# Kernel tuning notes

Hardware: AMD Instinct MI355X
Metric: run time of the kernel (lower is better)

## Reference

```python
import jax, jax.numpy as jnp
import numpy as np

N, IN_C, HID, OUT_C, DEPTH = 4096, 128, 256, 128, 3
KS = [2048, 1024, 512]  # ceil(0.5 * N_level)
E = 131072


def glorot(key, fan_in, fan_out):
    lim = np.sqrt(6.0 / (fan_in + fan_out))
    return jax.random.uniform(key, (fan_in, fan_out), jnp.float32, -lim, lim)


def build_adj(edge_index, n):
    # symmetric, self-loop-free adjacency with unit edge weights
    A = jnp.zeros((n, n), jnp.float32)
    A = A.at[edge_index[0], edge_index[1]].set(1.0)
    A = jnp.maximum(A, A.T)
    return A * (1.0 - jnp.eye(n, dtype=jnp.float32))


def gcn(x, A, W, b):
    # GCNConv(improved=True): A_hat = A + 2I, symmetric normalization
    n = A.shape[0]
    Ah = A + 2.0 * jnp.eye(n, dtype=A.dtype)
    deg = Ah.sum(axis=1)
    dinv = jnp.where(deg > 0, deg ** -0.5, 0.0)
    An = dinv[:, None] * Ah * dinv[None, :]
    return An @ (x @ W) + b


def augment(A):
    # remove self loops, add self loops (w=1), square (spspmm), remove self loops
    n = A.shape[0]
    I = jnp.eye(n, dtype=A.dtype)
    Al = A * (1.0 - I) + I
    A2 = Al @ Al
    return A2 * (1.0 - I)


def topk_pool(x, A, p, k):
    score = jnp.tanh((x @ p) / jnp.linalg.norm(p))
    vals, perm = jax.lax.top_k(score, k)
    return x[perm] * vals[:, None], A[perm][:, perm], perm


def setup_inputs() -> dict:
    key = jax.random.key(0)
    ks = jax.random.split(key, 16)
    x = jax.random.normal(ks[0], (N, IN_C), jnp.float32)
    edge_index = jax.random.randint(ks[1], (2, E), 0, N, jnp.int32)
    d = {"x": x, "edge_index": edge_index}
    d["Wd0"], d["bd0"] = glorot(ks[2], IN_C, HID), jnp.zeros((HID,), jnp.float32)
    d["Wd1"], d["bd1"] = glorot(ks[3], HID, HID), jnp.zeros((HID,), jnp.float32)
    d["Wd2"], d["bd2"] = glorot(ks[4], HID, HID), jnp.zeros((HID,), jnp.float32)
    d["Wd3"], d["bd3"] = glorot(ks[5], HID, HID), jnp.zeros((HID,), jnp.float32)
    d["p1"] = jax.random.normal(ks[6], (HID,), jnp.float32)
    d["p2"] = jax.random.normal(ks[7], (HID,), jnp.float32)
    d["p3"] = jax.random.normal(ks[8], (HID,), jnp.float32)
    d["Wu0"], d["bu0"] = glorot(ks[9], HID, HID), jnp.zeros((HID,), jnp.float32)
    d["Wu1"], d["bu1"] = glorot(ks[10], HID, HID), jnp.zeros((HID,), jnp.float32)
    d["Wu2"], d["bu2"] = glorot(ks[11], HID, OUT_C), jnp.zeros((OUT_C,), jnp.float32)
    return d


def reference(x, edge_index, Wd0, bd0, Wd1, bd1, Wd2, bd2, Wd3, bd3,
              p1, p2, p3, Wu0, bu0, Wu1, bu1, Wu2, bu2):
    n = x.shape[0]
    A = build_adj(edge_index, n)
    x = jax.nn.relu(gcn(x, A, Wd0, bd0))
    xs, As, perms = [x], [A], []
    down = [(Wd1, bd1), (Wd2, bd2), (Wd3, bd3)]
    pools = [p1, p2, p3]
    for i in range(DEPTH):
        A = augment(A)
        x, A, perm = topk_pool(x, A, pools[i], KS[i])
        x = jax.nn.relu(gcn(x, A, *down[i]))
        if i < DEPTH - 1:
            xs.append(x)
            As.append(A)
        perms.append(perm)
    up = [(Wu0, bu0), (Wu1, bu1), (Wu2, bu2)]
    for i in range(DEPTH):
        j = DEPTH - 1 - i
        res, perm = xs[j], perms[j]
        u = jnp.zeros_like(res).at[perm].set(x)
        x = res + u  # sum_res=True
        x = gcn(x, As[j], *up[i])
        if i < DEPTH - 1:
            x = jax.nn.relu(x)
    return x
```

## Files before the change

### kernel.cpp

```cpp
#include <hip/hip_runtime.h>


typedef __attribute__((ext_vector_type(8))) short bf16x8;
typedef __attribute__((ext_vector_type(4))) short s16x4;
typedef __attribute__((ext_vector_type(4))) float f32x4;

__device__ __forceinline__ short f2bf(float f) {
    unsigned u = __builtin_bit_cast(unsigned, f);
    u += 0x7FFFu + ((u >> 16) & 1u);
    return (short)(u >> 16);
}
__device__ __forceinline__ float bf2f(short s) {
    unsigned u = ((unsigned)(unsigned short)s) << 16;
    return __builtin_bit_cast(float, u);
}

#define GLL16(gsrc, ldst)                                                        \
    __builtin_amdgcn_global_load_lds(                                            \
        (__attribute__((address_space(1))) void*)(gsrc),                         \
        (__attribute__((address_space(3))) void*)(ldst), 16, 0, 0)

template<int MODE, int EPI>
__global__ __launch_bounds__(256, 2)
void gemm_bt(const short* __restrict__ Ah, const short* __restrict__ Al,
             const short* __restrict__ Bh, const short* __restrict__ Bl,
             float* __restrict__ Cf, int M, int N, int K, int kChunk)
{
    if (EPI == 1 && (int)blockIdx.y > (int)blockIdx.x) return;

    __shared__ short sAh[128 * 32];
    __shared__ short sBh[128 * 32];
    __shared__ short sAl[(MODE == 2) ? 128 * 32 : 8];
    __shared__ short sBl[(MODE >= 1) ? 128 * 32 : 8];

    const int t    = threadIdx.x;
    const int lane = t & 63;
    const int wave = t >> 6;
    const int tM   = blockIdx.y * 128;
    const int tN   = blockIdx.x * 128;
    const int k0   = blockIdx.z * kChunk;

    const int wm  = (wave >> 1) * 64;
    const int wn  = (wave & 1) * 64;
    const int l15 = lane & 15;
    const int g8  = (lane >> 4) * 8;

    f32x4 acc[4][4];
    const f32x4 zero = {0.f, 0.f, 0.f, 0.f};
#pragma unroll
    for (int i = 0; i < 4; i++)
#pragma unroll
        for (int j = 0; j < 4; j++) acc[i][j] = zero;

    const int i0 = t, i1 = t + 256;
    const short* a0 = Ah + (size_t)(tM + (i0 >> 2)) * K + (i0 & 3) * 8;
    const short* a1 = Ah + (size_t)(tM + (i1 >> 2)) * K + (i1 & 3) * 8;
    const short* b0 = Bh + (size_t)(tN + (i0 >> 2)) * K + (i0 & 3) * 8;
    const short* b1 = Bh + (size_t)(tN + (i1 >> 2)) * K + (i1 & 3) * 8;
    const short *bl0 = nullptr, *bl1 = nullptr, *al0 = nullptr, *al1 = nullptr;
    if (MODE >= 1) {
        bl0 = Bl + (size_t)(tN + (i0 >> 2)) * K + (i0 & 3) * 8;
        bl1 = Bl + (size_t)(tN + (i1 >> 2)) * K + (i1 & 3) * 8;
    }
    if (MODE == 2) {
        al0 = Al + (size_t)(tM + (i0 >> 2)) * K + (i0 & 3) * 8;
        al1 = Al + (size_t)(tM + (i1 >> 2)) * K + (i1 & 3) * 8;
    }

    for (int kb = k0; kb < k0 + kChunk; kb += 32) {
        GLL16(a0 + kb, &sAh[i0 * 8]);
        GLL16(a1 + kb, &sAh[i1 * 8]);
        GLL16(b0 + kb, &sBh[i0 * 8]);
        GLL16(b1 + kb, &sBh[i1 * 8]);
        if (MODE >= 1) { GLL16(bl0 + kb, &sBl[i0 * 8]); GLL16(bl1 + kb, &sBl[i1 * 8]); }
        if (MODE == 2) { GLL16(al0 + kb, &sAl[i0 * 8]); GLL16(al1 + kb, &sAl[i1 * 8]); }
        __syncthreads();

        bf16x8 aF[4], bF[4], aL[4], bL[4];
#pragma unroll
        for (int i = 0; i < 4; i++)
            aF[i] = *(const bf16x8*)&sAh[(wm + i * 16 + l15) * 32 + g8];
#pragma unroll
        for (int j = 0; j < 4; j++)
            bF[j] = *(const bf16x8*)&sBh[(wn + j * 16 + l15) * 32 + g8];
        if (MODE >= 1)
#pragma unroll
            for (int j = 0; j < 4; j++)
                bL[j] = *(const bf16x8*)&sBl[(wn + j * 16 + l15) * 32 + g8];
        if (MODE == 2)
#pragma unroll
            for (int i = 0; i < 4; i++)
                aL[i] = *(const bf16x8*)&sAl[(wm + i * 16 + l15) * 32 + g8];

#pragma unroll
        for (int i = 0; i < 4; i++)
#pragma unroll
            for (int j = 0; j < 4; j++) {
                acc[i][j] = __builtin_amdgcn_mfma_f32_16x16x32_bf16(aF[i], bF[j], acc[i][j], 0, 0, 0);
                if (MODE >= 1)
                    acc[i][j] = __builtin_amdgcn_mfma_f32_16x16x32_bf16(aF[i], bL[j], acc[i][j], 0, 0, 0);
                if (MODE == 2)
                    acc[i][j] = __builtin_amdgcn_mfma_f32_16x16x32_bf16(aL[i], bF[j], acc[i][j], 0, 0, 0);
            }
        __syncthreads();
    }

    const int r4 = (lane >> 4) * 4;
    if (EPI == 3) {
        float* CT = Cf + (size_t)blockIdx.z * M * N;
#pragma unroll
        for (int i = 0; i < 4; i++)
#pragma unroll
            for (int j = 0; j < 4; j++) {
                const int col   = tN + wn + j * 16 + l15;
                const int rbase = tM + wm + i * 16 + r4;
                *(f32x4*)&CT[(size_t)col * M + rbase] = acc[i][j];
            }
    } else {
        float* Cg = Cf + (size_t)blockIdx.z * M * N;
#pragma unroll
        for (int i = 0; i < 4; i++)
#pragma unroll
            for (int j = 0; j < 4; j++) {
                const int col = tN + wn + j * 16 + l15;
                float* cp = Cg + (size_t)(tM + wm + i * 16 + r4) * N + col;
#pragma unroll
                for (int r = 0; r < 4; r++) cp[(size_t)r * N] = acc[i][j][r];
            }
        if (EPI == 1 && tM != tN) {
#pragma unroll
            for (int i = 0; i < 4; i++)
#pragma unroll
                for (int j = 0; j < 4; j++) {
                    const int col   = tN + wn + j * 16 + l15;
                    const int rbase = tM + wm + i * 16 + r4;
                    *(f32x4*)&Cg[(size_t)col * N + rbase] = acc[i][j];
                }
        }
    }
}


__global__ void prep(const float* __restrict__ Wd0, const float* __restrict__ Wd1,
                     const float* __restrict__ Wd2, const float* __restrict__ Wd3,
                     const float* __restrict__ Wu0, const float* __restrict__ Wu1,
                     const float* __restrict__ Wu2, const float* __restrict__ x0,
                     short* __restrict__ Wth, short* __restrict__ Wtl,
                     short* __restrict__ Xh, short* __restrict__ Xl,
                     unsigned long long* __restrict__ M0)
{
    int t = blockIdx.x * 256 + threadIdx.x;
    float v; int dst;
    if (t < 32768)       { int e = t;          v = Wd0[e]; dst = 0      + (e & 255) * 128 + (e >> 8); }
    else if (t < 98304)  { int e = t - 32768;  v = Wd1[e]; dst = 32768  + (e & 255) * 256 + (e >> 8); }
    else if (t < 163840) { int e = t - 98304;  v = Wd2[e]; dst = 98304  + (e & 255) * 256 + (e >> 8); }
    else if (t < 229376) { int e = t - 163840; v = Wd3[e]; dst = 163840 + (e & 255) * 256 + (e >> 8); }
    else if (t < 294912) { int e = t - 229376; v = Wu0[e]; dst = 229376 + (e & 255) * 256 + (e >> 8); }
    else if (t < 360448) { int e = t - 294912; v = Wu1[e]; dst = 294912 + (e & 255) * 256 + (e >> 8); }
    else if (t < 393216) { int e = t - 360448; v = Wu2[e]; dst = 360448 + (e & 127) * 256 + (e >> 7); }
    else if (t < 917504) {
        int e = t - 393216;
        v = x0[e];
        short h = f2bf(v);
        Xh[e] = h; Xl[e] = f2bf(v - bf2f(h));
        return;
    } else {
        M0[t - 917504] = 0ull;
        return;
    }
    short h = f2bf(v);
    Wth[dst] = h; Wtl[dst] = f2bf(v - bf2f(h));
}

__global__ void build_bits(const int* __restrict__ ei, int E,
                           unsigned long long* __restrict__ M0)
{
    int e = blockIdx.x * 256 + threadIdx.x;
    if (e >= E) return;
    int i = ei[e], j = ei[E + e];
    if (i != j) {
        atomicOr(&M0[(size_t)i * 64 + (j >> 6)], 1ull << (j & 63));
        atomicOr(&M0[(size_t)j * 64 + (i >> 6)], 1ull << (i & 63));
    }
}

__global__ void row_compact_bits(const unsigned long long* __restrict__ M0,
                                 int* __restrict__ csr, float* __restrict__ rs)
{
    int row = blockIdx.x * 4 + (threadIdx.x >> 6);
    int lane = threadIdx.x & 63;
    unsigned long long w = M0[(size_t)row * 64 + lane];
    int c = __popcll(w);
    int incl = c;
    for (int off = 1; off < 64; off <<= 1) {
        int v = __shfl_up(incl, off);
        if (lane >= off) incl += v;
    }
    int base = incl - c;
    int* out = csr + (size_t)row * 128;
    while (w) {
        int b = __ffsll((unsigned long long)w) - 1;
        if (base < 128) out[base] = lane * 64 + b;
        base++;
        w &= w - 1;
    }
    if (lane == 63) rs[row] = (float)incl;
}

__global__ void mask_gather(const unsigned long long* __restrict__ M0,
                            const int* __restrict__ perm,
                            unsigned long long* __restrict__ mask,
                            float* __restrict__ rs, int kk)
{
    int t = blockIdx.x * 256 + threadIdx.x;
    if (t < kk) rs[t] = 0.f;
    int r = t >> 6, l = t & 63;
    int u = perm[r];
    unsigned long long w = M0[(size_t)u * 64 + l];
    if ((u >> 6) == l) w |= 1ull << (u & 63);
    mask[t] = w;
}

#define PSTR2 18
__global__ __launch_bounds__(256, 8)
void popc_aug_p(const unsigned long long* __restrict__ mask,
                short* __restrict__ Cp)
{
    const int bx = blockIdx.x, by = blockIdx.y, z = blockIdx.z;
    if (by > bx) return;
    __shared__ unsigned long long a[64 * PSTR2];
    __shared__ unsigned long long b[64 * PSTR2];
    const int t = threadIdx.x;
#pragma unroll
    for (int p = 0; p < 4; p++) {
        int idx = p * 256 + t;
        int rr = idx >> 4, w = idx & 15;
        a[rr * PSTR2 + w] = mask[((size_t)(by * 64 + rr)) * 64 + z * 16 + w];
        b[rr * PSTR2 + w] = mask[((size_t)(bx * 64 + rr)) * 64 + z * 16 + w];
    }
    __syncthreads();
    const int i0 = (t >> 4) * 4;
    const int j0 = t & 15;
    int acc[4][4];
#pragma unroll
    for (int qi = 0; qi < 4; qi++)
#pragma unroll
        for (int qj = 0; qj < 4; qj++) acc[qi][qj] = 0;
#pragma unroll
    for (int w = 0; w < 16; w += 2) {
        ulong2 av[4], bv[4];
#pragma unroll
        for (int q = 0; q < 4; q++) av[q] = *(const ulong2*)&a[(i0 + q) * PSTR2 + w];
#pragma unroll
        for (int q = 0; q < 4; q++) bv[q] = *(const ulong2*)&b[(j0 + 16 * q) * PSTR2 + w];
#pragma unroll
        for (int qi = 0; qi < 4; qi++)
#pragma unroll
            for (int qj = 0; qj < 4; qj++) {
                acc[qi][qj] += __builtin_popcountll(av[qi].x & bv[qj].x);
                acc[qi][qj] += __builtin_popcountll(av[qi].y & bv[qj].y);
            }
    }
    short* out = Cp + ((size_t)z * 1024 + (size_t)(by * 32 + bx)) * 4096;
#pragma unroll
    for (int qi = 0; qi < 4; qi++)
#pragma unroll
        for (int qj = 0; qj < 4; qj++)
            out[(i0 + qi) * 64 + j0 + 16 * qj] = (short)acc[qi][qj];
}

__global__ __launch_bounds__(256)
void aug_merge(const short* __restrict__ Cp, int kk,
               short* __restrict__ Ahs, float* __restrict__ rs)
{
    const int bx = blockIdx.x, by = blockIdx.y;
    if (by > bx) return;
    __shared__ float tile[64][65];
    __shared__ float rsum[64], csum[64];
    const int t = threadIdx.x;
    const int i  = t >> 2;
    const int c0 = (t & 3) * 16;
    const size_t tb = (size_t)(by * 32 + bx) * 4096;
    const size_t ss = (size_t)1024 * 4096;
    if (t < 64) { rsum[t] = 0.f; csum[t] = 0.f; }

    int v[16];
#pragma unroll
    for (int q = 0; q < 16; q++) v[q] = 0;
    for (int s = 0; s < 4; s++) {
        bf16x8 p0 = *(const bf16x8*)&Cp[tb + s * ss + i * 64 + c0];
        bf16x8 p1 = *(const bf16x8*)&Cp[tb + s * ss + i * 64 + c0 + 8];
#pragma unroll
        for (int q = 0; q < 8; q++) { v[q] += (int)p0[q]; v[8 + q] += (int)p1[q]; }
    }
    const int gi = by * 64 + i;
    float rp = 0.f;
    s16x4 pk[4];
#pragma unroll
    for (int q = 0; q < 16; q++) {
        const int gj = bx * 64 + c0 + q;
        float val = (gi == gj) ? 0.f : (float)v[q];
        tile[i][c0 + q] = val;
        rp += val;
        pk[q >> 2][q & 3] = f2bf(val);
    }
#pragma unroll
    for (int q = 0; q < 4; q++)
        *(s16x4*)&Ahs[(size_t)gi * kk + bx * 64 + c0 + q * 4] = pk[q];
    __syncthreads();
    atomicAdd(&rsum[i], rp);
    if (bx != by) {
        float cpv = 0.f;
#pragma unroll
        for (int q = 0; q < 16; q++) {
            float val = tile[c0 + q][i];
            cpv += val;
            pk[q >> 2][q & 3] = f2bf(val);
        }
#pragma unroll
        for (int q = 0; q < 4; q++)
            *(s16x4*)&Ahs[(size_t)(bx * 64 + i) * kk + by * 64 + c0 + q * 4] = pk[q];
        atomicAdd(&csum[i], cpv);
    }
    __syncthreads();
    if (t < 64) {
        atomicAdd(&rs[by * 64 + t], rsum[t]);
        if (bx != by) atomicAdd(&rs[bx * 64 + t], csum[t]);
    }
}

__global__ void z_reduce(const float* __restrict__ Cp, int S,
                         const float* __restrict__ rs,
                         short* __restrict__ Zh, short* __restrict__ Zl,
                         int n, int C)
{
    int t4 = (blockIdx.x * 256 + threadIdx.x) * 4;
    int r = t4 % n;
    size_t stride = (size_t)n * C;
    f32x4 v = {0.f, 0.f, 0.f, 0.f};
    for (int s = 0; s < S; s++) v += *(const f32x4*)&Cp[t4 + s * stride];
    f32x4 rsv = *(const f32x4*)&rs[r];
    s16x4 zh, zl;
#pragma unroll
    for (int q = 0; q < 4; q++) {
        float z = v[q] / sqrtf(rsv[q] + 2.f);
        short h = f2bf(z);
        zh[q] = h; zl[q] = f2bf(z - bf2f(h));
    }
    *(s16x4*)&Zh[t4] = zh;
    *(s16x4*)&Zl[t4] = zl;
}

__global__ void zf_reduce(const float* __restrict__ Cp, int S,
                          const float* __restrict__ rs,
                          float* __restrict__ Zf, int n, int C)
{
    int t4 = (blockIdx.x * 256 + threadIdx.x) * 4;
    int r = t4 / C;
    size_t stride = (size_t)n * C;
    f32x4 v = {0.f, 0.f, 0.f, 0.f};
    for (int s = 0; s < S; s++) v += *(const f32x4*)&Cp[t4 + s * stride];
    float d = 1.f / sqrtf(rs[r] + 2.f);
    v *= d;
    *(f32x4*)&Zf[t4] = v;
}

template<int CN, int RELU>
__global__ __launch_bounds__(256)
void spmm_gcn(const int* __restrict__ csr, const float* __restrict__ rs,
              const float* __restrict__ Zf, const float* __restrict__ b,
              float* __restrict__ out)
{
    const int lane = threadIdx.x & 63;
    const int row  = blockIdx.x * 4 + (threadIdx.x >> 6);
    const int dg   = (int)rs[row];
    const int* nb  = csr + (size_t)row * 128;
    if (CN == 256) {
        const int c = lane * 4;
        float4 acc = {0.f, 0.f, 0.f, 0.f};
        int q = 0;
        for (; q + 4 <= dg; q += 4) {
            int j0 = nb[q], j1 = nb[q+1], j2 = nb[q+2], j3 = nb[q+3];
            float4 z0 = *(const float4*)&Zf[(size_t)j0 * CN + c];
            float4 z1 = *(const float4*)&Zf[(size_t)j1 * CN + c];
            float4 z2 = *(const float4*)&Zf[(size_t)j2 * CN + c];
            float4 z3 = *(const float4*)&Zf[(size_t)j3 * CN + c];
            acc.x += z0.x; acc.y += z0.y; acc.z += z0.z; acc.w += z0.w;
            acc.x += z1.x; acc.y += z1.y; acc.z += z1.z; acc.w += z1.w;
            acc.x += z2.x; acc.y += z2.y; acc.z += z2.z; acc.w += z2.w;
            acc.x += z3.x; acc.y += z3.y; acc.z += z3.z; acc.w += z3.w;
        }
        for (; q < dg; q++) {
            float4 z = *(const float4*)&Zf[(size_t)nb[q] * CN + c];
            acc.x += z.x; acc.y += z.y; acc.z += z.z; acc.w += z.w;
        }
        float d = 1.f / sqrtf(rs[row] + 2.f);
        float4 zi = *(const float4*)&Zf[(size_t)row * CN + c];
        float4 bb = *(const float4*)&b[c];
        float4 g;
        g.x = d * acc.x + 2.f * d * zi.x + bb.x;
        g.y = d * acc.y + 2.f * d * zi.y + bb.y;
        g.z = d * acc.z + 2.f * d * zi.z + bb.z;
        g.w = d * acc.w + 2.f * d * zi.w + bb.w;
        if (RELU) {
            g.x = fmaxf(g.x, 0.f); g.y = fmaxf(g.y, 0.f);
            g.z = fmaxf(g.z, 0.f); g.w = fmaxf(g.w, 0.f);
        }
        *(float4*)&out[(size_t)row * CN + c] = g;
    } else {
        const int c = lane * 2;
        float2 acc = {0.f, 0.f};
        int q = 0;
        for (; q + 4 <= dg; q += 4) {
            int j0 = nb[q], j1 = nb[q+1], j2 = nb[q+2], j3 = nb[q+3];
            float2 z0 = *(const float2*)&Zf[(size_t)j0 * CN + c];
            float2 z1 = *(const float2*)&Zf[(size_t)j1 * CN + c];
            float2 z2 = *(const float2*)&Zf[(size_t)j2 * CN + c];
            float2 z3 = *(const float2*)&Zf[(size_t)j3 * CN + c];
            acc.x += z0.x; acc.y += z0.y;
            acc.x += z1.x; acc.y += z1.y;
            acc.x += z2.x; acc.y += z2.y;
            acc.x += z3.x; acc.y += z3.y;
        }
        for (; q < dg; q++) {
            float2 z = *(const float2*)&Zf[(size_t)nb[q] * CN + c];
            acc.x += z.x; acc.y += z.y;
        }
        float d = 1.f / sqrtf(rs[row] + 2.f);
        float2 zi = *(const float2*)&Zf[(size_t)row * CN + c];
        float2 g;
        g.x = d * acc.x + 2.f * d * zi.x + b[c];
        g.y = d * acc.y + 2.f * d * zi.y + b[c + 1];
        if (RELU) { g.x = fmaxf(g.x, 0.f); g.y = fmaxf(g.y, 0.f); }
        *(float2*)&out[(size_t)row * CN + c] = g;
    }
}

__global__ void gcn_final(const float* __restrict__ Cp, int S,
                          const short* __restrict__ Zh, const short* __restrict__ Zl,
                          const float* __restrict__ rs, const float* __restrict__ b,
                          float* __restrict__ out, short* __restrict__ oh,
                          short* __restrict__ ol, int k, int C, int relu,
                          const int* __restrict__ inv, const float* __restrict__ res)
{
    int t4 = (blockIdx.x * 256 + threadIdx.x) * 4;
    int j = t4 / C, c = t4 - j * C;
    int r = inv ? inv[j] : j;
    f32x4 v = res ? *(const f32x4*)&res[t4] : (f32x4){0.f, 0.f, 0.f, 0.f};
    if (r >= 0) {
        size_t base = (size_t)r * C + c;
        size_t stride = (size_t)k * C;
        f32x4 az = {0.f, 0.f, 0.f, 0.f};
        for (int s = 0; s < S; s++) az += *(const f32x4*)&Cp[base + s * stride];
        float d = 1.f / sqrtf(rs[r] + 2.f);
        f32x4 bb = *(const f32x4*)&b[c];
#pragma unroll
        for (int q = 0; q < 4; q++) {
            size_t zi = (size_t)(c + q) * k + r;
            float zz = bf2f(Zh[zi]) + bf2f(Zl[zi]);
            float g = d * az[q] + 2.f * d * zz + bb[q];
            if (relu && g < 0.f) g = 0.f;
            v[q] += g;
        }
    }
    *(f32x4*)&out[t4] = v;
    if (oh) {
        s16x4 hh, ll;
#pragma unroll
        for (int q = 0; q < 4; q++) {
            short h = f2bf(v[q]);
            hh[q] = h; ll[q] = f2bf(v[q] - bf2f(h));
        }
        *(s16x4*)&oh[t4] = hh;
        *(s16x4*)&ol[t4] = ll;
    }
}

__global__ void score_kernel(const float* __restrict__ x,
                             const float* __restrict__ p,
                             float* __restrict__ score, int n,
                             int* __restrict__ rankb)
{
    int row = blockIdx.x * 4 + (threadIdx.x >> 6);
    int lane = threadIdx.x & 63;
    float4 pv = ((const float4*)p)[lane];
    float4 xv = ((const float4*)(x + (size_t)row * 256))[lane];
    double nn  = (double)pv.x * pv.x + (double)pv.y * pv.y +
                 (double)pv.z * pv.z + (double)pv.w * pv.w;
    double acc = (double)xv.x * pv.x + (double)xv.y * pv.y +
                 (double)xv.z * pv.z + (double)xv.w * pv.w;
    for (int off = 32; off; off >>= 1) {
        acc += __shfl_down(acc, off);
        nn  += __shfl_down(nn, off);
    }
    if (lane == 0) {
        score[row] = tanhf((float)(acc / sqrt(nn)));
        rankb[row] = 0;
    }
}

__device__ __forceinline__ unsigned long long packkey(float s, int i) {
    unsigned u = __builtin_bit_cast(unsigned, s);
    u = (u & 0x80000000u) ? ~u : (u | 0x80000000u);
    return ((unsigned long long)u << 32) | (unsigned)(0xFFFFFFFFu - (unsigned)i);
}

__global__ __launch_bounds__(256)
void rank_count(const float* __restrict__ score,
                int* __restrict__ rankb)
{
    __shared__ unsigned long long sk[256];
    int i = blockIdx.x * 256 + threadIdx.x;
    int j = blockIdx.y * 256 + threadIdx.x;
    sk[threadIdx.x] = packkey(score[j], j);
    unsigned long long mykey = packkey(score[i], i);
    __syncthreads();
    int part = 0;
#pragma unroll 16
    for (int q = 0; q < 256; q++) part += (sk[q] > mykey) ? 1 : 0;
    atomicAdd(&rankb[i], part);
}

__global__ void rank_final(const float* __restrict__ score,
                           const int* __restrict__ rankb, int k,
                           int* __restrict__ perm, float* __restrict__ vals,
                           int* __restrict__ inv)
{
    int i = blockIdx.x * 256 + threadIdx.x;
    int rank = rankb[i];
    if (rank < k) { perm[rank] = i; vals[rank] = score[i]; }
    inv[i] = (rank < k) ? rank : -1;
}

__global__ void gather_x_hl(const float* __restrict__ xold,
                            const int* __restrict__ perm,
                            const float* __restrict__ vals,
                            short* __restrict__ Xh, short* __restrict__ Xl, int C)
{
    int t4 = (blockIdx.x * 256 + threadIdx.x) * 4;
    int r = t4 / C, c = t4 - r * C;
    float vv = vals[r];
    f32x4 x = *(const f32x4*)&xold[(size_t)perm[r] * C + c];
    s16x4 hh, ll;
#pragma unroll
    for (int q = 0; q < 4; q++) {
        float v = x[q] * vv;
        short h = f2bf(v);
        hh[q] = h; ll[q] = f2bf(v - bf2f(h));
    }
    *(s16x4*)&Xh[t4] = hh;
    *(s16x4*)&Xl[t4] = ll;
}

__global__ void gatherG_h(const short* __restrict__ A, int n,
                          const int* __restrict__ perm,
                          short* __restrict__ Gh, int kk,
                          float* __restrict__ rsz)
{
    int idx = blockIdx.x * 256 + threadIdx.x;
    if (idx < kk) rsz[idx] = 0.f;
    int t8 = idx * 8;
    if (t8 >= kk * n) return;
    int r = t8 / n, c0 = t8 - r * n;
    int pr = perm[r];
    bf16x8 a = *(const bf16x8*)&A[(size_t)pr * n + c0];
    if (pr >= c0 && pr < c0 + 8)
        a[pr - c0] = f2bf(bf2f(a[pr - c0]) + 1.f);
    *(bf16x8*)&Gh[t8] = a;
}

__global__ void gatherG_hl(const short* __restrict__ Ahi, const short* __restrict__ Alo,
                           int n, const int* __restrict__ perm,
                           short* __restrict__ Gh, short* __restrict__ Gl, int kk,
                           float* __restrict__ rsz)
{
    int idx = blockIdx.x * 256 + threadIdx.x;
    if (idx < kk) rsz[idx] = 0.f;
    int t8 = idx * 8;
    if (t8 >= kk * n) return;
    int r = t8 / n, c0 = t8 - r * n;
    int pr = perm[r];
    bf16x8 ah = *(const bf16x8*)&Ahi[(size_t)pr * n + c0];
    bf16x8 al = *(const bf16x8*)&Alo[(size_t)pr * n + c0];
    bf16x8 gh, gl;
#pragma unroll
    for (int q = 0; q < 8; q++) {
        float v = bf2f(ah[q]) + bf2f(al[q]) + ((c0 + q == pr) ? 1.f : 0.f);
        short h = f2bf(v);
        gh[q] = h; gl[q] = f2bf(v - bf2f(h));
    }
    *(bf16x8*)&Gh[t8] = gh;
    *(bf16x8*)&Gl[t8] = gl;
}

template<bool LO>
__global__ void aug_finish_f(const float* __restrict__ Cp, int S, int kk,
                             short* __restrict__ Ahs, short* __restrict__ Als,
                             float* __restrict__ rs)
{
    int t4 = (blockIdx.x * 256 + threadIdx.x) * 4;
    int r = t4 / kk, c0 = t4 - r * kk;
    size_t stride = (size_t)kk * kk;
    f32x4 v = {0.f, 0.f, 0.f, 0.f};
    for (int s = 0; s < S; s++) v += *(const f32x4*)&Cp[t4 + s * stride];
    if (r >= c0 && r < c0 + 4) v[r - c0] = 0.f;
    s16x4 hh, ll;
    float ws = 0.f;
#pragma unroll
    for (int q = 0; q < 4; q++) {
        short h = f2bf(v[q]);
        hh[q] = h;
        if (LO) ll[q] = f2bf(v[q] - bf2f(h));
        ws += v[q];
    }
    *(s16x4*)&Ahs[t4] = hh;
    if (LO) *(s16x4*)&Als[t4] = ll;
    for (int off = 32; off; off >>= 1) ws += __shfl_down(ws, off);
    if ((threadIdx.x & 63) == 0) atomicAdd(&rs[r], ws);
}


extern "C" void kernel_launch(void* const* d_in, const int* in_sizes, int n_in,
                              void* d_out, int out_size, void* d_ws, size_t ws_size,
                              hipStream_t stream)
{
    const float* x0  = (const float*)d_in[0];
    const int*   ei  = (const int*)d_in[1];
    const float* Wd0 = (const float*)d_in[2];  const float* bd0 = (const float*)d_in[3];
    const float* Wd1 = (const float*)d_in[4];  const float* bd1 = (const float*)d_in[5];
    const float* Wd2 = (const float*)d_in[6];  const float* bd2 = (const float*)d_in[7];
    const float* Wd3 = (const float*)d_in[8];  const float* bd3 = (const float*)d_in[9];
    const float* p1  = (const float*)d_in[10];
    const float* p2  = (const float*)d_in[11];
    const float* p3  = (const float*)d_in[12];
    const float* Wu0 = (const float*)d_in[13]; const float* bu0 = (const float*)d_in[14];
    const float* Wu1 = (const float*)d_in[15]; const float* bu1 = (const float*)d_in[16];
    const float* Wu2 = (const float*)d_in[17]; const float* bu2 = (const float*)d_in[18];

    const int E = in_sizes[1] / 2;

    char* ws = (char*)d_ws;
    size_t off = 0;
    auto alloc = [&](size_t bytes) -> void* {
        void* p = ws + off;
        off += (bytes + 255) & ~(size_t)255;
        return p;
    };
    unsigned long long* M0 = (unsigned long long*)alloc((size_t)4096 * 64 * 8);
    short* A1h  = (short*)alloc((size_t)2048 * 2048 * 2);
    short* A2h  = (short*)alloc((size_t)1024 * 1024 * 2);
    short* A2l  = (short*)alloc((size_t)1024 * 1024 * 2);
    short* A3h  = (short*)alloc((size_t)512 * 512 * 2);
    short* A3l  = (short*)alloc((size_t)512 * 512 * 2);
    short* Gh   = (short*)alloc((size_t)1024 * 2048 * 2);
    short* Gl   = (short*)alloc((size_t)512 * 1024 * 2);
    int*   csr  = (int*)alloc((size_t)4096 * 128 * 4);
    unsigned long long* maskb = (unsigned long long*)alloc((size_t)2048 * 64 * 8);
    float* Zf   = (float*)alloc((size_t)4096 * 256 * 4);
    float* Cp   = (float*)alloc((size_t)64 * 1024 * 1024);
    float* xs0  = (float*)alloc((size_t)4096 * 256 * 4);
    float* xs1  = (float*)alloc((size_t)2048 * 256 * 4);
    float* xs2  = (float*)alloc((size_t)1024 * 256 * 4);
    float* xu0  = (float*)alloc((size_t)4096 * 256 * 4);
    float* xu1  = (float*)alloc((size_t)2048 * 256 * 4);
    float* xu2  = (float*)alloc((size_t)1024 * 256 * 4);
    short* xu0h = (short*)alloc((size_t)4096 * 256 * 2);
    short* xu0l = (short*)alloc((size_t)4096 * 256 * 2);
    short* xu1h = (short*)alloc((size_t)2048 * 256 * 2);
    short* xu1l = (short*)alloc((size_t)2048 * 256 * 2);
    short* xu2h = (short*)alloc((size_t)1024 * 256 * 2);
    short* xu2l = (short*)alloc((size_t)1024 * 256 * 2);
    short* X0h  = (short*)alloc((size_t)4096 * 128 * 2);
    short* X0l  = (short*)alloc((size_t)4096 * 128 * 2);
    short* xah  = (short*)alloc((size_t)2048 * 256 * 2);
    short* xal  = (short*)alloc((size_t)2048 * 256 * 2);
    short* Wth  = (short*)alloc((size_t)393216 * 2);
    short* Wtl  = (short*)alloc((size_t)393216 * 2);
    short* Zh   = (short*)alloc((size_t)256 * 4096 * 2);
    short* Zl   = (short*)alloc((size_t)256 * 4096 * 2);
    float* rs0  = (float*)alloc(4096 * 4);
    float* rs1  = (float*)alloc(2048 * 4);
    float* rs2  = (float*)alloc(1024 * 4);
    float* rs3  = (float*)alloc(512 * 4);
    float* scoreb = (float*)alloc(4096 * 4);
    float* valsb  = (float*)alloc(2048 * 4);
    int*   rankb  = (int*)alloc(4096 * 4);
    int*   perm1  = (int*)alloc(2048 * 4);
    int*   perm2  = (int*)alloc(1024 * 4);
    int*   perm3  = (int*)alloc(512 * 4);
    int*   inv1   = (int*)alloc(4096 * 4);
    int*   inv2   = (int*)alloc(2048 * 4);
    int*   inv3   = (int*)alloc(1024 * 4);

    auto gcn_dense = [&](const short* Xh, const short* Xl, int n, int Kc, int Cout,
                         const short* pAh, const short* pAl, const float* rsA,
                         int wtoff, const float* b,
                         float* out, short* oh, short* ol, int relu, int modeA,
                         int Saz, const int* inv, const float* res, int nout) {
        int Sxw = 4;
        gemm_bt<2, 3><<<dim3(Cout / 128, n / 128, Sxw), 256, 0, stream>>>(
            Xh, Xl, Wth + wtoff, Wtl + wtoff, Cp, n, Cout, Kc, Kc / Sxw);
        z_reduce<<<(n * Cout) / 1024, 256, 0, stream>>>(Cp, Sxw, rsA, Zh, Zl, n, Cout);
        dim3 g(Cout / 128, n / 128, Saz);
        if (modeA == 1)
            gemm_bt<1, 0><<<g, 256, 0, stream>>>(pAh, nullptr, Zh, Zl, Cp, n, Cout, n, n / Saz);
        else
            gemm_bt<2, 0><<<g, 256, 0, stream>>>(pAh, pAl, Zh, Zl, Cp, n, Cout, n, n / Saz);
        gcn_final<<<(nout * Cout) / 1024, 256, 0, stream>>>(
            Cp, Saz, Zh, Zl, rsA, b, out, oh, ol, n, Cout, relu, inv, res);
    };

    auto pool = [&](const float* xlev, int n, const float* p, int* perm, int* inv) {
        int k = n / 2;
        score_kernel<<<n / 4, 256, 0, stream>>>(xlev, p, scoreb, n, rankb);
        rank_count<<<dim3(n / 256, n / 256), 256, 0, stream>>>(scoreb, rankb);
        rank_final<<<n / 256, 256, 0, stream>>>(scoreb, rankb, k, perm, valsb, inv);
        gather_x_hl<<<k / 4, 256, 0, stream>>>(xlev, perm, valsb, xah, xal, 256);
    };

    prep<<<4608, 256, 0, stream>>>(Wd0, Wd1, Wd2, Wd3, Wu0, Wu1, Wu2, x0,
                                   Wth, Wtl, X0h, X0l, M0);
    build_bits<<<(E + 255) / 256, 256, 0, stream>>>(ei, E, M0);
    row_compact_bits<<<1024, 256, 0, stream>>>(M0, csr, rs0);

    gemm_bt<2, 0><<<dim3(2, 32, 4), 256, 0, stream>>>(
        X0h, X0l, Wth, Wtl, Cp, 4096, 256, 128, 32);
    zf_reduce<<<1024, 256, 0, stream>>>(Cp, 4, rs0, Zf, 4096, 256);
    spmm_gcn<256, 1><<<1024, 256, 0, stream>>>(csr, rs0, Zf, bd0, xs0);

    pool(xs0, 4096, p1, perm1, inv1);
    mask_gather<<<512, 256, 0, stream>>>(M0, perm1, maskb, rs1, 2048);
    popc_aug_p<<<dim3(32, 32, 4), 256, 0, stream>>>(maskb, (short*)Cp);
    aug_merge<<<dim3(32, 32), 256, 0, stream>>>((const short*)Cp, 2048, A1h, rs1);
    gcn_dense(xah, xal, 2048, 256, 256, A1h, nullptr, rs1, 32768, bd1,
              xs1, nullptr, nullptr, 1, 1, 8, nullptr, nullptr, 2048);

    pool(xs1, 2048, p2, perm2, inv2);
    gatherG_h<<<(1024 * 2048 / 8) / 256, 256, 0, stream>>>(A1h, 2048, perm2, Gh, 1024, rs2);
    gemm_bt<0, 1><<<dim3(8, 8, 8), 256, 0, stream>>>(Gh, nullptr, Gh, nullptr, Cp, 1024, 1024, 2048, 256);
    aug_finish_f<true><<<(1024 * 1024 / 4) / 256, 256, 0, stream>>>(Cp, 8, 1024, A2h, A2l, rs2);
    gcn_dense(xah, xal, 1024, 256, 256, A2h, A2l, rs2, 98304, bd2,
              xs2, nullptr, nullptr, 1, 2, 8, nullptr, nullptr, 1024);

    pool(xs2, 1024, p3, perm3, inv3);
    gatherG_hl<<<(512 * 1024 / 8) / 256, 256, 0, stream>>>(A2h, A2l, 1024, perm3, Gh, Gl, 512, rs3);
    gemm_bt<2, 1><<<dim3(4, 4, 8), 256, 0, stream>>>(Gh, Gl, Gh, Gl, Cp, 512, 512, 1024, 128);
    aug_finish_f<true><<<(512 * 512 / 4) / 256, 256, 0, stream>>>(Cp, 8, 512, A3h, A3l, rs3);

    gcn_dense(xah, xal, 512, 256, 256, A3h, A3l, rs3, 163840, bd3,
              xu2, xu2h, xu2l, 1, 2, 8, inv3, xs2, 1024);

    gcn_dense(xu2h, xu2l, 1024, 256, 256, A2h, A2l, rs2, 229376, bu0,
              xu1, xu1h, xu1l, 1, 2, 8, inv2, xs1, 2048);

    gcn_dense(xu1h, xu1l, 2048, 256, 256, A1h, nullptr, rs1, 294912, bu1,
              xu0, xu0h, xu0l, 1, 1, 8, inv1, xs0, 4096);

    gemm_bt<2, 0><<<dim3(1, 32, 8), 256, 0, stream>>>(
        xu0h, xu0l, Wth + 360448, Wtl + 360448, Cp, 4096, 128, 256, 32);
    zf_reduce<<<512, 256, 0, stream>>>(Cp, 8, rs0, Zf, 4096, 128);
    spmm_gcn<128, 0><<<1024, 256, 0, stream>>>(csr, rs0, Zf, bu2, (float*)d_out);
}
```

Measured before the change: 447.6 us.

## Fuse pooling score into GCN epilogues and merge rank/gather into one kernel

The tanh(x·p/|p|) score is now computed in the epilogue of the GCN kernel that produces each level's features (spmm_gcn and gcn_final), which removes the separate score kernel and a re-read of x. The rank-count, rank-final and gather kernels are merged into one rank_pool kernel. Each block ranks 64 nodes by scanning all scores through shared memory, then gathers and splits the selected rows into bf16 hi/lo parts. This cuts three kernel launches per pooling level and drops the rank/vals buffers and global atomics. The cost is that each block redundantly scans all n scores, and there are fewer blocks (n/64).

```diff
diff --git a/kernel.cpp b/kernel.cpp
--- a/kernel.cpp
+++ b/kernel.cpp
@@ -365,11 +365,12 @@
     *(f32x4*)&Zf[t4] = v;
 }
 
-template<int CN, int RELU>
+template<int CN, int RELU, int SC>
 __global__ __launch_bounds__(256)
 void spmm_gcn(const int* __restrict__ csr, const float* __restrict__ rs,
               const float* __restrict__ Zf, const float* __restrict__ b,
-              float* __restrict__ out)
+              float* __restrict__ out,
+              const float* __restrict__ pvec, float* __restrict__ score)
 {
     const int lane = threadIdx.x & 63;
     const int row  = blockIdx.x * 4 + (threadIdx.x >> 6);
@@ -407,6 +408,18 @@
             g.z = fmaxf(g.z, 0.f); g.w = fmaxf(g.w, 0.f);
         }
         *(float4*)&out[(size_t)row * CN + c] = g;
+        if (SC) {
+            float4 pv = ((const float4*)pvec)[lane];
+            double nn  = (double)pv.x * pv.x + (double)pv.y * pv.y +
+                         (double)pv.z * pv.z + (double)pv.w * pv.w;
+            double acd = (double)g.x * pv.x + (double)g.y * pv.y +
+                         (double)g.z * pv.z + (double)g.w * pv.w;
+            for (int off = 32; off; off >>= 1) {
+                acd += __shfl_down(acd, off);
+                nn  += __shfl_down(nn, off);
+            }
+            if (lane == 0) score[row] = tanhf((float)(acd / sqrt(nn)));
+        }
     } else {
         const int c = lane * 2;
         float2 acc = {0.f, 0.f};
@@ -441,7 +454,8 @@
                           const float* __restrict__ rs, const float* __restrict__ b,
                           float* __restrict__ out, short* __restrict__ oh,
                           short* __restrict__ ol, int k, int C, int relu,
-                          const int* __restrict__ inv, const float* __restrict__ res)
+                          const int* __restrict__ inv, const float* __restrict__ res,
+                          const float* __restrict__ pvec, float* __restrict__ score)
 {
     int t4 = (blockIdx.x * 256 + threadIdx.x) * 4;
     int j = t4 / C, c = t4 - j * C;
@@ -474,28 +488,18 @@
         *(s16x4*)&oh[t4] = hh;
         *(s16x4*)&ol[t4] = ll;
     }
-}
-
-__global__ void score_kernel(const float* __restrict__ x,
-                             const float* __restrict__ p,
-                             float* __restrict__ score, int n,
-                             int* __restrict__ rankb)
-{
-    int row = blockIdx.x * 4 + (threadIdx.x >> 6);
-    int lane = threadIdx.x & 63;
-    float4 pv = ((const float4*)p)[lane];
-    float4 xv = ((const float4*)(x + (size_t)row * 256))[lane];
-    double nn  = (double)pv.x * pv.x + (double)pv.y * pv.y +
-                 (double)pv.z * pv.z + (double)pv.w * pv.w;
-    double acc = (double)xv.x * pv.x + (double)xv.y * pv.y +
-                 (double)xv.z * pv.z + (double)xv.w * pv.w;
-    for (int off = 32; off; off >>= 1) {
-        acc += __shfl_down(acc, off);
-        nn  += __shfl_down(nn, off);
-    }
-    if (lane == 0) {
-        score[row] = tanhf((float)(acc / sqrt(nn)));
-        rankb[row] = 0;
+    if (pvec) {
+        const int lane = threadIdx.x & 63;
+        float4 pv = *(const float4*)&pvec[c];
+        double nn  = (double)pv.x * pv.x + (double)pv.y * pv.y +
+                     (double)pv.z * pv.z + (double)pv.w * pv.w;
+        double acd = (double)v[0] * pv.x + (double)v[1] * pv.y +
+                     (double)v[2] * pv.z + (double)v[3] * pv.w;
+        for (int off = 32; off; off >>= 1) {
+            acd += __shfl_down(acd, off);
+            nn  += __shfl_down(nn, off);
+        }
+        if (lane == 0) score[j] = tanhf((float)(acd / sqrt(nn)));
     }
 }
 
@@ -506,50 +510,64 @@
 }
 
 __global__ __launch_bounds__(256)
-void rank_count(const float* __restrict__ score,
-                int* __restrict__ rankb)
+void rank_pool(const float* __restrict__ score, int n, int k,
+               const float* __restrict__ xold,
+               int* __restrict__ perm, int* __restrict__ inv,
+               short* __restrict__ Xh, short* __restrict__ Xl)
 {
     __shared__ unsigned long long sk[256];
-    int i = blockIdx.x * 256 + threadIdx.x;
-    int j = blockIdx.y * 256 + threadIdx.x;
-    sk[threadIdx.x] = packkey(score[j], j);
-    unsigned long long mykey = packkey(score[i], i);
+    __shared__ int rk[64];
+    __shared__ int selrow[64];
+    __shared__ int selrank[64];
+    __shared__ float selval[64];
+    __shared__ int cnt;
+    const int t  = threadIdx.x;
+    const int il = t & 63;
+    const int js = t >> 6;
+    const int i  = blockIdx.x * 64 + il;
+    if (t < 64) rk[t] = 0;
+    if (t == 0) cnt = 0;
+    const unsigned long long mykey = packkey(score[i], i);
+    int r = 0;
+    for (int jb = 0; jb < n; jb += 256) {
+        __syncthreads();
+        sk[t] = packkey(score[jb + t], jb + t);
+        __syncthreads();
+        const unsigned long long* p = &sk[js * 64];
+#pragma unroll 16
+        for (int q = 0; q < 64; q++) r += (p[q] > mykey) ? 1 : 0;
+    }
+    atomicAdd(&rk[il], r);
     __syncthreads();
-    int part = 0;
-#pragma unroll 16
-    for (int q = 0; q < 256; q++) part += (sk[q] > mykey) ? 1 : 0;
-    atomicAdd(&rankb[i], part);
-}
-
-__global__ void rank_final(const float* __restrict__ score,
-                           const int* __restrict__ rankb, int k,
-                           int* __restrict__ perm, float* __restrict__ vals,
-                           int* __restrict__ inv)
-{
-    int i = blockIdx.x * 256 + threadIdx.x;
-    int rank = rankb[i];
-    if (rank < k) { perm[rank] = i; vals[rank] = score[i]; }
-    inv[i] = (rank < k) ? rank : -1;
-}
-
-__global__ void gather_x_hl(const float* __restrict__ xold,
-                            const int* __restrict__ perm,
-                            const float* __restrict__ vals,
-                            short* __restrict__ Xh, short* __restrict__ Xl, int C)
-{
-    int t4 = (blockIdx.x * 256 + threadIdx.x) * 4;
-    int r = t4 / C, c = t4 - r * C;
-    float vv = vals[r];
-    f32x4 x = *(const f32x4*)&xold[(size_t)perm[r] * C + c];
-    s16x4 hh, ll;
-#pragma unroll
-    for (int q = 0; q < 4; q++) {
-        float v = x[q] * vv;
-        short h = f2bf(v);
-        hh[q] = h; ll[q] = f2bf(v - bf2f(h));
-    }
-    *(s16x4*)&Xh[t4] = hh;
-    *(s16x4*)&Xl[t4] = ll;
+    if (t < 64) {
+        int rank = rk[t];
+        int ii = blockIdx.x * 64 + t;
+        inv[ii] = (rank < k) ? rank : -1;
+        if (rank < k) {
+            perm[rank] = ii;
+            int s = atomicAdd(&cnt, 1);
+            selrow[s]  = ii;
+            selrank[s] = rank;
+            selval[s]  = score[ii];
+        }
+    }
+    __syncthreads();
+    const int wave = t >> 6, lane = t & 63;
+    for (int s = wave; s < cnt; s += 4) {
+        const int   row = selrow[s];
+        const float vv  = selval[s];
+        f32x4 x = *(const f32x4*)&xold[(size_t)row * 256 + lane * 4];
+        s16x4 hh, ll;
+#pragma unroll
+        for (int q = 0; q < 4; q++) {
+            float v = x[q] * vv;
+            short h = f2bf(v);
+            hh[q] = h; ll[q] = f2bf(v - bf2f(h));
+        }
+        size_t o = (size_t)selrank[s] * 256 + lane * 4;
+        *(s16x4*)&Xh[o] = hh;
+        *(s16x4*)&Xl[o] = ll;
+    }
 }
 
 __global__ void gatherG_h(const short* __restrict__ A, int n,
@@ -683,8 +701,6 @@
     float* rs2  = (float*)alloc(1024 * 4);
     float* rs3  = (float*)alloc(512 * 4);
     float* scoreb = (float*)alloc(4096 * 4);
-    float* valsb  = (float*)alloc(2048 * 4);
-    int*   rankb  = (int*)alloc(4096 * 4);
     int*   perm1  = (int*)alloc(2048 * 4);
     int*   perm2  = (int*)alloc(1024 * 4);
     int*   perm3  = (int*)alloc(512 * 4);
@@ -696,7 +712,8 @@
                          const short* pAh, const short* pAl, const float* rsA,
                          int wtoff, const float* b,
                          float* out, short* oh, short* ol, int relu, int modeA,
-                         int Saz, const int* inv, const float* res, int nout) {
+                         int Saz, const int* inv, const float* res, int nout,
+                         const float* pvec) {
         int Sxw = 4;
         gemm_bt<2, 3><<<dim3(Cout / 128, n / 128, Sxw), 256, 0, stream>>>(
             Xh, Xl, Wth + wtoff, Wtl + wtoff, Cp, n, Cout, Kc, Kc / Sxw);
@@ -707,15 +724,13 @@
         else
             gemm_bt<2, 0><<<g, 256, 0, stream>>>(pAh, pAl, Zh, Zl, Cp, n, Cout, n, n / Saz);
         gcn_final<<<(nout * Cout) / 1024, 256, 0, stream>>>(
-            Cp, Saz, Zh, Zl, rsA, b, out, oh, ol, n, Cout, relu, inv, res);
+            Cp, Saz, Zh, Zl, rsA, b, out, oh, ol, n, Cout, relu, inv, res,
+            pvec, scoreb);
     };
 
-    auto pool = [&](const float* xlev, int n, const float* p, int* perm, int* inv) {
+    auto pool = [&](const float* xlev, int n, int* perm, int* inv) {
         int k = n / 2;
-        score_kernel<<<n / 4, 256, 0, stream>>>(xlev, p, scoreb, n, rankb);
-        rank_count<<<dim3(n / 256, n / 256), 256, 0, stream>>>(scoreb, rankb);
-        rank_final<<<n / 256, 256, 0, stream>>>(scoreb, rankb, k, perm, valsb, inv);
-        gather_x_hl<<<k / 4, 256, 0, stream>>>(xlev, perm, valsb, xah, xal, 256);
+        rank_pool<<<n / 64, 256, 0, stream>>>(scoreb, n, k, xlev, perm, inv, xah, xal);
     };
 
     prep<<<4608, 256, 0, stream>>>(Wd0, Wd1, Wd2, Wd3, Wu0, Wu1, Wu2, x0,
@@ -726,38 +741,39 @@
     gemm_bt<2, 0><<<dim3(2, 32, 4), 256, 0, stream>>>(
         X0h, X0l, Wth, Wtl, Cp, 4096, 256, 128, 32);
     zf_reduce<<<1024, 256, 0, stream>>>(Cp, 4, rs0, Zf, 4096, 256);
-    spmm_gcn<256, 1><<<1024, 256, 0, stream>>>(csr, rs0, Zf, bd0, xs0);
-
-    pool(xs0, 4096, p1, perm1, inv1);
+    spmm_gcn<256, 1, 1><<<1024, 256, 0, stream>>>(csr, rs0, Zf, bd0, xs0, p1, scoreb);
+
+    pool(xs0, 4096, perm1, inv1);
     mask_gather<<<512, 256, 0, stream>>>(M0, perm1, maskb, rs1, 2048);
     popc_aug_p<<<dim3(32, 32, 4), 256, 0, stream>>>(maskb, (short*)Cp);
     aug_merge<<<dim3(32, 32), 256, 0, stream>>>((const short*)Cp, 2048, A1h, rs1);
     gcn_dense(xah, xal, 2048, 256, 256, A1h, nullptr, rs1, 32768, bd1,
-              xs1, nullptr, nullptr, 1, 1, 8, nullptr, nullptr, 2048);
-
-    pool(xs1, 2048, p2, perm2, inv2);
+              xs1, nullptr, nullptr, 1, 1, 8, nullptr, nullptr, 2048, p2);
+
+    pool(xs1, 2048, perm2, inv2);
     gatherG_h<<<(1024 * 2048 / 8) / 256, 256, 0, stream>>>(A1h, 2048, perm2, Gh, 1024, rs2);
     gemm_bt<0, 1><<<dim3(8, 8, 8), 256, 0, stream>>>(Gh, nullptr, Gh, nullptr, Cp, 1024, 1024, 2048, 256);
     aug_finish_f<true><<<(1024 * 1024 / 4) / 256, 256, 0, stream>>>(Cp, 8, 1024, A2h, A2l, rs2);
     gcn_dense(xah, xal, 1024, 256, 256, A2h, A2l, rs2, 98304, bd2,
-              xs2, nullptr, nullptr, 1, 2, 8, nullptr, nullptr, 1024);
-
-    pool(xs2, 1024, p3, perm3, inv3);
+              xs2, nullptr, nullptr, 1, 2, 8, nullptr, nullptr, 1024, p3);
+
+    pool(xs2, 1024, perm3, inv3);
     gatherG_hl<<<(512 * 1024 / 8) / 256, 256, 0, stream>>>(A2h, A2l, 1024, perm3, Gh, Gl, 512, rs3);
     gemm_bt<2, 1><<<dim3(4, 4, 8), 256, 0, stream>>>(Gh, Gl, Gh, Gl, Cp, 512, 512, 1024, 128);
     aug_finish_f<true><<<(512 * 512 / 4) / 256, 256, 0, stream>>>(Cp, 8, 512, A3h, A3l, rs3);
 
     gcn_dense(xah, xal, 512, 256, 256, A3h, A3l, rs3, 163840, bd3,
-              xu2, xu2h, xu2l, 1, 2, 8, inv3, xs2, 1024);
+              xu2, xu2h, xu2l, 1, 2, 8, inv3, xs2, 1024, nullptr);
 
     gcn_dense(xu2h, xu2l, 1024, 256, 256, A2h, A2l, rs2, 229376, bu0,
-              xu1, xu1h, xu1l, 1, 2, 8, inv2, xs1, 2048);
+              xu1, xu1h, xu1l, 1, 2, 8, inv2, xs1, 2048, nullptr);
 
     gcn_dense(xu1h, xu1l, 2048, 256, 256, A1h, nullptr, rs1, 294912, bu1,
-              xu0, xu0h, xu0l, 1, 1, 8, inv1, xs0, 4096);
+              xu0, xu0h, xu0l, 1, 1, 8, inv1, xs0, 4096, nullptr);
 
     gemm_bt<2, 0><<<dim3(1, 32, 8), 256, 0, stream>>>(
         xu0h, xu0l, Wth + 360448, Wtl + 360448, Cp, 4096, 128, 256, 32);
     zf_reduce<<<512, 256, 0, stream>>>(Cp, 8, rs0, Zf, 4096, 128);
-    spmm_gcn<128, 0><<<1024, 256, 0, stream>>>(csr, rs0, Zf, bu2, (float*)d_out);
-}
+    spmm_gcn<128, 0, 0><<<1024, 256, 0, stream>>>(csr, rs0, Zf, bu2, (float*)d_out,
+                                                  nullptr, nullptr);
+}
```

After: 460.2 us. 2.8% more time.
